# Kernel tuning notes

Measured on AMD Instinct MI355X. Metric: run time of the kernel, lower is better.

Reference implementation:

```python
import jax, jax.numpy as jnp
import numpy as np

N_NODES = 50000
N_EDGES = 600000
N_GRAPHS = 512
HID = 128
LAT = 64
L = 4
BN_EPS = 1e-5


def _gelu(x):
    return jax.nn.gelu(x, approximate=False)


def _bn(x, g, b):
    m = jnp.mean(x, axis=0)
    v = jnp.var(x, axis=0)
    return (x - m) * jax.lax.rsqrt(v + BN_EPS) * g + b


def setup_inputs() -> dict:
    key = jax.random.key(0)
    ks = jax.random.split(key, 8)
    x = jax.random.normal(ks[0], (N_NODES, HID), dtype=jnp.float32)
    edge_index = jax.random.randint(ks[1], (2, N_EDGES), 0, N_NODES, dtype=jnp.int64 if jax.config.jax_enable_x64 else jnp.int32)
    batch = jnp.sort(jax.random.randint(ks[2], (N_NODES,), 0, N_GRAPHS))
    scale = 1.0 / np.sqrt(HID)
    return {
        "x": x,
        "edge_index": edge_index,
        "batch": batch,
        "input_bn_g": jnp.ones((HID,), jnp.float32),
        "input_bn_b": jnp.zeros((HID,), jnp.float32),
        "eps": jnp.zeros((L,), jnp.float32),
        "fc1_w": jax.random.normal(ks[3], (L, HID, HID), jnp.float32) * scale,
        "fc1_b": jnp.zeros((L, HID), jnp.float32),
        "bn1_g": jnp.ones((L, HID), jnp.float32),
        "bn1_b": jnp.zeros((L, HID), jnp.float32),
        "fc2_w": jax.random.normal(ks[4], (L, HID, HID), jnp.float32) * scale,
        "fc2_b": jnp.zeros((L, HID), jnp.float32),
        "bn_g": jnp.ones((L, HID), jnp.float32),
        "bn_b": jnp.zeros((L, HID), jnp.float32),
        "att_weight": jax.random.normal(ks[5], (L, HID), jnp.float32),
        "pool_weight": jnp.ones((3,), jnp.float32),
        "fcA_w": jax.random.normal(ks[6], (HID, HID), jnp.float32) * scale,
        "fcA_b": jnp.zeros((HID,), jnp.float32),
        "ln_g": jnp.ones((HID,), jnp.float32),
        "ln_b": jnp.zeros((HID,), jnp.float32),
        "fcB_w": jax.random.normal(ks[7], (HID, LAT), jnp.float32) * scale,
        "fcB_b": jnp.zeros((LAT,), jnp.float32),
    }


def reference(x, edge_index, batch, input_bn_g, input_bn_b, eps, fc1_w, fc1_b,
              bn1_g, bn1_b, fc2_w, fc2_b, bn_g, bn_b, att_weight, pool_weight,
              fcA_w, fcA_b, ln_g, ln_b, fcB_w, fcB_b):
    src, dst = edge_index[0], edge_index[1]
    x = _bn(x, input_bn_g, input_bn_b)  # input BatchNorm (batch stats)
    hidden_states = []
    for l in range(L):
        # GINConv: (1+eps)*x_i + sum_{j->i} x_j, then GatedResidualMLP
        agg = jax.ops.segment_sum(x[src], dst, num_segments=N_NODES)
        h = (1.0 + eps[l]) * x + agg
        h = _gelu(_bn(h @ fc1_w[l] + fc1_b[l], bn1_g[l], bn1_b[l]))
        h = h @ fc2_w[l] + fc2_b[l]
        h = _gelu(_bn(h, bn_g[l], bn_b[l]))
        hidden_states.append(h)
        x = h
    # JumpingKnowledge attention over layers
    x_all = jnp.stack(hidden_states, axis=0)               # [L, N, H]
    scores = jnp.mean(x_all * att_weight[:, None, :], -1)  # [L, N]
    alpha = jax.nn.softmax(scores, axis=0)
    x = jnp.sum(x_all * alpha[..., None], axis=0)          # [N, H]
    # fused add/mean/max pooling by graph id
    pw = jax.nn.softmax(pool_weight)
    sums = jax.ops.segment_sum(x, batch, num_segments=N_GRAPHS)
    cnt = jax.ops.segment_sum(jnp.ones((N_NODES, 1), x.dtype), batch, num_segments=N_GRAPHS)
    mean = sums / jnp.maximum(cnt, 1.0)
    mx = jax.ops.segment_max(x, batch, num_segments=N_GRAPHS)
    mx = jnp.where(cnt > 0, mx, 0.0)
    pooled = sums * pw[0] + mean * pw[1] + mx * pw[2]      # [G, H]
    out = pooled @ fcA_w + fcA_b
    mu = jnp.mean(out, -1, keepdims=True)
    var = jnp.var(out, -1, keepdims=True)
    out = (out - mu) * jax.lax.rsqrt(var + 1e-5) * ln_g + ln_b
    out = _gelu(out) + pooled
    return out @ fcB_w + fcB_b                              # [G, latent]
```

## Files before the change

### kernel.cpp

```cpp
#include <hip/hip_runtime.h>
#include <math.h>

#define N_NODES 50000
#define N_EDGES 600000
#define N_GRAPHS 512
#define HID 128
#define LAT 64
#define NL 4
#define SSTR 16
#define NGRP 16
#define PSET (NGRP * 256 * SSTR)
#define N_TILES 3125
#define ZROWS 208
#define ZLD 136

typedef __attribute__((ext_vector_type(8))) __bf16 bf16x8;
typedef __attribute__((ext_vector_type(4))) float f32x4;

union Chunk {
    bf16x8 v;
    uint4 u4;
    ushort us[8];
};

// ... 138 lines not shown
    } else {
        int n = (bx - 2600) * 256 + t;
        if (n < N_NODES) {
            int b = batch[n];
            if (n == 0 || batch[n - 1] != b) gstart[b] = n;
            if (n == N_NODES - 1 || batch[n + 1] != b) gend[b] = n + 1;
        }
    }
}

__global__ __launch_bounds__(256) void bn_scan(const float* __restrict__ X,
                                               ushort* __restrict__ Y,
                                               const float* __restrict__ inPart,
                                               const float* __restrict__ g,
                                               const float* __restrict__ b,
                                               const int* __restrict__ counts,
                                               int* __restrict__ offs,
                                               int* __restrict__ bsum) {
    __shared__ float scL[HID], sfL[HID];
    __shared__ int shI[256];
    int t = threadIdx.x;
    if (t < HID) {
        float sm = 0.f, sq = 0.f;
#pragma unroll
        for (int gg = 0; gg < NGRP; ++gg) {
            sm += inPart[((long)gg * 256 + t) * SSTR];
            sq += inPart[((long)gg * 256 + HID + t) * SSTR];
        }
        const float invN = 1.0f / (float)N_NODES;
        float mean = sm * invN;
        float var = sq * invN - mean * mean;
        float s = g[t] * rsqrtf(var + 1e-5f);
        scL[t] = s;
        sfL[t] = b[t] - mean * s;
    }
    __syncthreads();
    int c4 = (t & 31) * 4;
    float sc[4], sf[4];
#pragma unroll
    for (int j = 0; j < 4; ++j) { sc[j] = scL[c4 + j]; sf[j] = sfL[c4 + j]; }
    int s0, s1;
    sub_range(blockIdx.x & 255, blockIdx.x >> 8, s0, s1);
    int c0 = s0 * 32, c1 = s1 * 32;
    for (int i = c0 + t; i < c1; i += 256) {
        float4 v = ((const float4*)X)[i];
        ushort4 w;
        w.x = f2bf(v.x * sc[0] + sf[0]);
        w.y = f2bf(v.y * sc[1] + sf[1]);
        w.z = f2bf(v.z * sc[2] + sf[2]);
        w.w = f2bf(v.w * sc[3] + sf[3]);
        ((ushort4*)Y)[i] = w;
    }
    if (blockIdx.x < 196) {
        int i = blockIdx.x * 256 + t;
        int v = (i < N_NODES) ? counts[i] : 0;
        shI[t] = v;
        __syncthreads();
        for (int off = 1; off < 256; off <<= 1) {
            int a = (t >= off) ? shI[t - off] : 0;
            __syncthreads();
            shI[t] += a;
            __syncthreads();
        }
        if (i < N_NODES) offs[i] = shI[t] - v;
        if (t == 255) bsum[blockIdx.x] = shI[255];
    }
}

__global__ __launch_bounds__(256) void scan23(int* __restrict__ offs,
                                              const int* __restrict__ bsum,
                                              int* __restrict__ cursor) {
    __shared__ int sh[256];
    int t = threadIdx.x, bx = blockIdx.x;
    int v = (t < bx) ? bsum[t] : 0;
    sh[t] = v;
    __syncthreads();
    for (int off = 128; off > 0; off >>= 1) {
        if (t < off) sh[t] += sh[t + off];
        __syncthreads();
    }
    int pre = sh[0];
    int i = bx * 256 + t;
    if (i < N_NODES) {
        int o = offs[i] + pre;
        offs[i] = o;
        cursor[i] = o;
    }
}

__global__ __launch_bounds__(256) void csr_fill(const int* __restrict__ src,
                                                const int* __restrict__ dst,
                                                int* __restrict__ cursor,
                                                int* __restrict__ csr) {
    int e = blockIdx.x * blockDim.x + threadIdx.x;
    if (e >= N_EDGES) return;
    int pos = atomicAdd(cursor + dst[e], 1);
    csr[pos] = src[e];
}

__global__ __launch_bounds__(256) void gin_gather_bf(const ushort* __restrict__ Xbf,
                                                     ushort* __restrict__ Hp,
                                                     const int* __restrict__ offs,
                                                     const int* __restrict__ counts,
                                                     const int* __restrict__ csr,
                                                     const float* __restrict__ eps, int l) {
    int t = threadIdx.x;
    int tx = t & 31;
    int grp = t >> 5;
    int s0, s1;
    sub_range(blockIdx.x & 255, blockIdx.x >> 8, s0, s1);
    float ev = 1.0f + eps[l];
    for (int node = s0 + grp; node < s1; node += 8) {
        ushort4 sv = *(const ushort4*)(Xbf + (long)node * HID + 4 * tx);
        float a0 = bf2f(sv.x) * ev, a1 = bf2f(sv.y) * ev;
        float a2 = bf2f(sv.z) * ev, a3 = bf2f(sv.w) * ev;
        int o = offs[node];
        int d = counts[node];
        int k = 0;
        for (; k + 8 <= d; k += 8) {
            int si[8];
#pragma unroll
            for (int j = 0; j < 8; ++j) si[j] = csr[o + k + j];
            ushort4 v[8];
#pragma unroll
            for (int j = 0; j < 8; ++j)
                v[j] = *(const ushort4*)(Xbf + (long)si[j] * HID + 4 * tx);
#pragma unroll
            for (int j = 0; j < 8; ++j) {
                a0 += bf2f(v[j].x); a1 += bf2f(v[j].y);
                a2 += bf2f(v[j].z); a3 += bf2f(v[j].w);
            }
        }
        for (; k + 4 <= d; k += 4) {
            int si[4];
#pragma unroll
            for (int j = 0; j < 4; ++j) si[j] = csr[o + k + j];
#pragma unroll
            for (int j = 0; j < 4; ++j) {
                ushort4 v = *(const ushort4*)(Xbf + (long)si[j] * HID + 4 * tx);
                a0 += bf2f(v.x); a1 += bf2f(v.y); a2 += bf2f(v.z); a3 += bf2f(v.w);
            }
        }
        for (; k < d; ++k) {
            int s = csr[o + k];
            ushort4 v = *(const ushort4*)(Xbf + (long)s * HID + 4 * tx);
            a0 += bf2f(v.x); a1 += bf2f(v.y); a2 += bf2f(v.z); a3 += bf2f(v.w);
        }
        ushort4 w;
        w.x = f2bf(a0); w.y = f2bf(a1); w.z = f2bf(a2); w.w = f2bf(a3);
        *(ushort4*)(Hp + (long)node * HID + 4 * tx) = w;
    }
}

template <int NT>
__global__ __launch_bounds__(NT, 1) void fused_mlp(
    const ushort* __restrict__ Abf, const ushort* __restrict__ W1t,
    const ushort* __restrict__ W2t, const float* __restrict__ b1v,
    const float* __restrict__ b2v, const float* __restrict__ bn1g,
    const float* __restrict__ bn1b, const float* __restrict__ bn2g,
    const float* __restrict__ bn2b, float* __restrict__ st1,
    float* __restrict__ st2, ushort* __restrict__ Hl, int* __restrict__ bar,
    int nbar) {
    constexpr int NW = NT / 64;
    constexpr int RSTEP = NW / 2;
    __shared__ __align__(16) ushort Z1[ZROWS * ZLD];
    __shared__ __align__(16) ushort Z2[ZROWS * ZLD];
    __shared__ float shs[2 * NT];
    __shared__ float scL[HID], sfL[HID];

    int t = threadIdx.x;
    int w = t >> 6, lane = t & 63;
    int m = lane & 15, q = lane >> 4;
    int c2 = w & 1, r2 = w >> 1;
    int t0 = (blockIdx.x * N_TILES) >> 8;
    int t1 = ((blockIdx.x + 1) * N_TILES) >> 8;
    int grp = blockIdx.x & (NGRP - 1);

    bf16x8 Bf[4][4];
    {
        const ushort* Wh = W1t + (long)(c2 * 64) * HID;
#pragma unroll
        for (int nt = 0; nt < 4; ++nt)
#pragma unroll
            for (int kc = 0; kc < 4; ++kc)
                Bf[nt][kc] = *(const bf16x8*)(Wh + (nt * 16 + m) * HID + kc * 32 + q * 8);
    }
    float bias4[4];
#pragma unroll
    for (int nt = 0; nt < 4; ++nt) bias4[nt] = b1v[c2 * 64 + nt * 16 + m];

    float s_c[4] = {0, 0, 0, 0}, q_c[4] = {0, 0, 0, 0};
    int tile = t0 + r2;
    Chunk Ac[4];
    if (tile < t1) {
        const ushort* ar = Abf + (long)(tile * 16 + m) * HID + q * 8;
#pragma unroll
        for (int kc = 0; kc < 4; ++kc) Ac[kc].u4 = *(const uint4*)(ar + kc * 32);
    }
    while (tile < t1) {
        int nxt = tile + RSTEP;
        Chunk An[4];
        if (nxt < t1) {
            const ushort* ar = Abf + (long)(nxt * 16 + m) * HID + q * 8;
#pragma unroll
            for (int kc = 0; kc < 4; ++kc) An[kc].u4 = *(const uint4*)(ar + kc * 32);
        }
        f32x4 acc[4];
#pragma unroll
        for (int nt = 0; nt < 4; ++nt) acc[nt] = (f32x4){0.f, 0.f, 0.f, 0.f};
#pragma unroll
        for (int kc = 0; kc < 4; ++kc)
#pragma unroll
            for (int nt = 0; nt < 4; ++nt)
                acc[nt] = __builtin_amdgcn_mfma_f32_16x16x32_bf16(Ac[kc].v, Bf[nt][kc],
                                                                  acc[nt], 0, 0, 0);
        int lrow = (tile - t0) * 16;
#pragma unroll
        for (int nt = 0; nt < 4; ++nt) {
            int col = c2 * 64 + nt * 16 + m;
#pragma unroll
            for (int r = 0; r < 4; ++r) {
                float z = acc[nt][r] + bias4[nt];
                Z1[(lrow + q * 4 + r) * ZLD + col] = f2bf(z);
                s_c[nt] += z;
                q_c[nt] += z * z;
            }
        }
        tile = nxt;
#pragma unroll
        for (int kc = 0; kc < 4; ++kc) Ac[kc] = An[kc];
    }
#pragma unroll
    for (int nt = 0; nt < 4; ++nt) {
        s_c[nt] += __shfl_xor(s_c[nt], 16);
        s_c[nt] += __shfl_xor(s_c[nt], 32);
        q_c[nt] += __shfl_xor(q_c[nt], 16);
        q_c[nt] += __shfl_xor(q_c[nt], 32);
    }
    if (q == 0) {
#pragma unroll
        for (int nt = 0; nt < 4; ++nt) {
            shs[w * 64 + nt * 16 + m] = s_c[nt];
            shs[NT + w * 64 + nt * 16 + m] = q_c[nt];
        }
    }
    __syncthreads();
    if (t < HID) {
        int half = t >> 6, lc = t & 63;
        float a = 0.f, b = 0.f;
#pragma unroll
        for (int j = 0; j < RSTEP; ++j) {
            a += shs[(half + 2 * j) * 64 + lc];
            b += shs[NT + (half + 2 * j) * 64 + lc];
        }
        float* base = st1 + (long)(grp * 256) * SSTR;
        atomicAdd(base + t * SSTR, a);
        atomicAdd(base + (HID + t) * SSTR, b);
    }
    for (int k = 0; k < nbar; ++k) grid_sync(bar, k + 1);

    if (t < HID) {
        float sm = 0.f, sq = 0.f;
#pragma unroll
        for (int gg = 0; gg < NGRP; ++gg) {
            sm += coh_ld(st1 + ((long)gg * 256 + t) * SSTR);
            sq += coh_ld(st1 + ((long)gg * 256 + HID + t) * SSTR);
        }
        const float invN = 1.0f / (float)N_NODES;
        float mean = sm * invN;
        float var = sq * invN - mean * mean;
        float s = bn1g[t] * rsqrtf(var + 1e-5f);
        scL[t] = s;
        sfL[t] = bn1b[t] - mean * s;
    }
    __syncthreads();

    {
        const ushort* Wh = W2t + (long)(c2 * 64) * HID;
#pragma unroll
        for (int nt = 0; nt < 4; ++nt)
#pragma unroll
            for (int kc = 0; kc < 4; ++kc)
                Bf[nt][kc] = *(const bf16x8*)(Wh + (nt * 16 + m) * HID + kc * 32 + q * 8);
    }
#pragma unroll
    for (int nt = 0; nt < 4; ++nt) bias4[nt] = b2v[c2 * 64 + nt * 16 + m];
#pragma unroll
    for (int nt = 0; nt < 4; ++nt) { s_c[nt] = 0.f; q_c[nt] = 0.f; }

    for (int tl = t0 + r2; tl < t1; tl += RSTEP) {
        int lrow = (tl - t0) * 16;
        Chunk Ax[4];
#pragma unroll
        for (int kc = 0; kc < 4; ++kc)
            Ax[kc].u4 = *(const uint4*)(Z1 + (lrow + m) * ZLD + kc * 32 + q * 8);
#pragma unroll
        for (int kc = 0; kc < 4; ++kc)
#pragma unroll
            for (int j = 0; j < 8; ++j) {
                int k = kc * 32 + q * 8 + j;
                float f = bf2f(Ax[kc].us[j]) * scL[k] + sfL[k];
                Ax[kc].us[j] = f2bf(gelu_fast(f));
            }
        f32x4 acc[4];
#pragma unroll
        for (int nt = 0; nt < 4; ++nt) acc[nt] = (f32x4){0.f, 0.f, 0.f, 0.f};
#pragma unroll
        for (int kc = 0; kc < 4; ++kc)
#pragma unroll
            for (int nt = 0; nt < 4; ++nt)
                acc[nt] = __builtin_amdgcn_mfma_f32_16x16x32_bf16(Ax[kc].v, Bf[nt][kc],
                                                                  acc[nt], 0, 0, 0);
#pragma unroll
        for (int nt = 0; nt < 4; ++nt) {
            int col = c2 * 64 + nt * 16 + m;
#pragma unroll
            for (int r = 0; r < 4; ++r) {
                float z = acc[nt][r] + bias4[nt];
                Z2[(lrow + q * 4 + r) * ZLD + col] = f2bf(z);
                s_c[nt] += z;
                q_c[nt] += z * z;
            }
        }
    }
#pragma unroll
    for (int nt = 0; nt < 4; ++nt) {
        s_c[nt] += __shfl_xor(s_c[nt], 16);
        s_c[nt] += __shfl_xor(s_c[nt], 32);
        q_c[nt] += __shfl_xor(q_c[nt], 16);
        q_c[nt] += __shfl_xor(q_c[nt], 32);
    }
    if (q == 0) {
#pragma unroll
        for (int nt = 0; nt < 4; ++nt) {
            shs[w * 64 + nt * 16 + m] = s_c[nt];
            shs[NT + w * 64 + nt * 16 + m] = q_c[nt];
        }
    }
    __syncthreads();
    if (t < HID) {
        int half = t >> 6, lc = t & 63;
        float a = 0.f, b = 0.f;
#pragma unroll
        for (int j = 0; j < RSTEP; ++j) {
            a += shs[(half + 2 * j) * 64 + lc];
            b += shs[NT + (half + 2 * j) * 64 + lc];
        }
        float* base = st2 + (long)(grp * 256) * SSTR;
        atomicAdd(base + t * SSTR, a);
        atomicAdd(base + (HID + t) * SSTR, b);
    }
    for (int k = 0; k < nbar; ++k) grid_sync(bar, nbar + k + 1);

    if (t < HID) {
        float sm = 0.f, sq = 0.f;
#pragma unroll
        for (int gg = 0; gg < NGRP; ++gg) {
            sm += coh_ld(st2 + ((long)gg * 256 + t) * SSTR);
            sq += coh_ld(st2 + ((long)gg * 256 + HID + t) * SSTR);
        }
        const float invN = 1.0f / (float)N_NODES;
        float mean = sm * invN;
        float var = sq * invN - mean * mean;
        float s = bn2g[t] * rsqrtf(var + 1e-5f);
        scL[t] = s;
        sfL[t] = bn2b[t] - mean * s;
    }
    __syncthreads();

    int nch = (t1 - t0) * 16 * 16;
    for (int i = t; i < nch; i += NT) {
        int row = i >> 4, off = i & 15;
        Chunk ch;
        ch.u4 = *(const uint4*)(Z2 + row * ZLD + off * 8);
#pragma unroll
        for (int j = 0; j < 8; ++j) {
            int cc = off * 8 + j;
            float f = bf2f(ch.us[j]) * scL[cc] + sfL[cc];
            ch.us[j] = f2bf(gelu_fast(f));
        }
        *(uint4*)(Hl + (long)(t0 * 16 + row) * HID + off * 8) = ch.u4;
    }
}

__global__ __launch_bounds__(256) void jk_pool(const ushort* __restrict__ H0,
                                               const ushort* __restrict__ H1,
                                               const ushort* __restrict__ H2,
                                               const ushort* __restrict__ H3,
                                               const float* __restrict__ att,
                                               const int* __restrict__ batch,
                                               float* __restrict__ psum,
                                               float* __restrict__ pmax) {
    int t = threadIdx.x;
    int lane = t & 63, w = t >> 6;
    long wid = (long)blockIdx.x * 4 + w;
    int a0 = (int)((wid * N_NODES) >> 13);
    int a1 = (int)(((wid + 1) * N_NODES) >> 13);
    const ushort* Hs[4] = {H0, H1, H2, H3};
    float2 av[4];
#pragma unroll
    for (int l = 0; l < 4; ++l) av[l] = *(const float2*)(att + l * HID + 2 * lane);

    int curg = -1;
    float sx = 0.f, sy = 0.f, mx = -INFINITY, my = -INFINITY;
    for (int node = a0; node < a1; ++node) {
        int g = batch[node];
        if (g != curg) {
            if (curg >= 0) {
                float* ps = psum + (long)curg * HID + 2 * lane;
                float* pm = pmax + (long)curg * HID + 2 * lane;
                atomicAdd(ps, sx);
                atomicAdd(ps + 1, sy);
                atomicMaxF(pm, mx);
                atomicMaxF(pm + 1, my);
            }
            curg = g;
            sx = 0.f; sy = 0.f; mx = -INFINITY; my = -INFINITY;
        }
        float hx[4], hy[4], scr[4];
#pragma unroll
        for (int l = 0; l < 4; ++l) {
            unsigned int u = *(const unsigned int*)(Hs[l] + (long)node * HID + 2 * lane);
            float vx = bf2f((ushort)(u & 0xFFFF));
            float vy = bf2f((ushort)(u >> 16));
            hx[l] = vx; hy[l] = vy;
            float p = vx * av[l].x + vy * av[l].y;
#pragma unroll
            for (int off = 32; off > 0; off >>= 1) p += __shfl_xor(p, off);
            scr[l] = p * (1.0f / HID);
        }
        float mm = fmaxf(fmaxf(scr[0], scr[1]), fmaxf(scr[2], scr[3]));
        float e[4], se = 0.f;
#pragma unroll
        for (int l = 0; l < 4; ++l) { e[l] = expf(scr[l] - mm); se += e[l]; }
        float inv = 1.0f / se;
        float ox = 0.f, oy = 0.f;
#pragma unroll
        for (int l = 0; l < 4; ++l) {
            float a = e[l] * inv;
            ox += a * hx[l];
            oy += a * hy[l];
        }
        sx += ox; sy += oy;
        mx = fmaxf(mx, ox); my = fmaxf(my, oy);
    }
    if (curg >= 0) {
        float* ps = psum + (long)curg * HID + 2 * lane;
        float* pm = pmax + (long)curg * HID + 2 * lane;
        atomicAdd(ps, sx);
        atomicAdd(ps + 1, sy);
        atomicMaxF(pm, mx);
        atomicMaxF(pm + 1, my);
    }
}

__global__ __launch_bounds__(128) void finalize_head(const float* __restrict__ psum,
                                                     const float* __restrict__ pmax,
                                                     const int* __restrict__ gstart,
                                                     const int* __restrict__ gend,
                                                     const float* __restrict__ pw,
                                                     const float* __restrict__ fcAw,
                                                     const float* __restrict__ fcAb,
                                                     const float* __restrict__ lng,
                                                     const float* __restrict__ lnb,
                                                     const float* __restrict__ fcBw,
                                                     const float* __restrict__ fcBb,
                                                     float* __restrict__ out) {
    __shared__ float p[HID], qv[HID], red[HID];
    int g = blockIdx.x, j = threadIdx.x;
    float w0 = pw[0], w1 = pw[1], w2 = pw[2];
    float mw = fmaxf(w0, fmaxf(w1, w2));
    float e0 = expf(w0 - mw), e1 = expf(w1 - mw), e2 = expf(w2 - mw);
    float inv = 1.0f / (e0 + e1 + e2);
    e0 *= inv; e1 *= inv; e2 *= inv;
    int cnt = gend[g] - gstart[g];
    float s = psum[g * HID + j];
    float mx = pmax[g * HID + j];
    float mean0 = cnt > 0 ? s / (float)cnt : 0.f;
    float mxv = cnt > 0 ? mx : 0.f;
    float pool = s * e0 + mean0 * e1 + mxv * e2;
    p[j] = pool;
    __syncthreads();
    float acc = fcAb[j];
    for (int k = 0; k < HID; ++k) acc += p[k] * fcAw[k * HID + j];
    red[j] = acc;
    __syncthreads();
    for (int off = 64; off > 0; off >>= 1) {
        if (j < off) red[j] += red[j + off];
        __syncthreads();
    }
    float mean = red[0] * (1.0f / HID);
    __syncthreads();
    float d = acc - mean;
    red[j] = d * d;
    __syncthreads();
    for (int off = 64; off > 0; off >>= 1) {
        if (j < off) red[j] += red[j + off];
        __syncthreads();
    }
    float var = red[0] * (1.0f / HID);
    float y = d * rsqrtf(var + 1e-5f) * lng[j] + lnb[j];
    qv[j] = gelu_exact(y) + pool;
    __syncthreads();
    if (j < LAT) {
        float o = fcBb[j];
        for (int k = 0; k < HID; ++k) o += qv[k] * fcBw[k * LAT + j];
        out[g * LAT + j] = o;
    }
}

extern "C" void kernel_launch(void* const* d_in, const int* in_sizes, int n_in,
                              void* d_out, int out_size, void* d_ws, size_t ws_size,
                              hipStream_t stream) {
    const float* x = (const float*)d_in[0];
    const int* ei = (const int*)d_in[1];
    const int* src = ei;
    const int* dst = ei + N_EDGES;
    const int* batch = (const int*)d_in[2];
    const float* ibn_g = (const float*)d_in[3];
    const float* ibn_b = (const float*)d_in[4];
    const float* eps = (const float*)d_in[5];
    const float* fc1w = (const float*)d_in[6];
    const float* fc1b = (const float*)d_in[7];
    const float* bn1g = (const float*)d_in[8];
    const float* bn1b = (const float*)d_in[9];
    const float* fc2w = (const float*)d_in[10];
    const float* fc2b = (const float*)d_in[11];
    const float* bng = (const float*)d_in[12];
    const float* bnb = (const float*)d_in[13];
    const float* att = (const float*)d_in[14];
    const float* pw = (const float*)d_in[15];
    const float* fcAw = (const float*)d_in[16];
    const float* fcAb = (const float*)d_in[17];
    const float* lng = (const float*)d_in[18];
    const float* lnb = (const float*)d_in[19];
    const float* fcBw = (const float*)d_in[20];
    const float* fcBb = (const float*)d_in[21];
    float* out = (float*)d_out;

    const size_t NH = (size_t)N_NODES * HID;
    char* w8 = (char*)d_ws;
    ushort* x0bf = (ushort*)w8;     w8 += NH * 2;
    ushort* hprebf = (ushort*)w8;   w8 += NH * 2;
    ushort* Hlbf[NL];
    for (int l = 0; l < NL; ++l) { Hlbf[l] = (ushort*)w8; w8 += NH * 2; }
    float* statsPart = (float*)w8;  w8 += (size_t)9 * PSET * 4;
    float* psum = (float*)w8;       w8 += (size_t)N_GRAPHS * HID * 4;
    float* pmax = (float*)w8;       w8 += (size_t)N_GRAPHS * HID * 4;
    int* gstart = (int*)w8;         w8 += N_GRAPHS * 4;
    int* gend = (int*)w8;           w8 += N_GRAPHS * 4;
    int* counts = (int*)w8;         w8 += N_NODES * 4;
    int* offs = (int*)w8;           w8 += N_NODES * 4;
    int* cursor = (int*)w8;         w8 += N_NODES * 4;
    int* bsum = (int*)w8;           w8 += 256 * 4;
    int* csr = (int*)w8;            w8 += (size_t)N_EDGES * 4;
    ushort* WtBf = (ushort*)w8;     w8 += (size_t)8 * HID * HID * 2;
    int* bar = (int*)w8;            w8 += 2048 * 4;

    const int edgeBlocks = (N_EDGES + 255) / 256;

    setup<<<512, 256, 0, stream>>>(fc1w, fc2w, WtBf, counts, statsPart,
                                   psum, pmax, gstart, gend, bar);
    stats_count<<<256 + edgeBlocks + 196, 256, 0, stream>>>(x, statsPart, dst, counts,
                                                            batch, gstart, gend);
    bn_scan<<<2048, 256, 0, stream>>>(x, x0bf, statsPart, ibn_g, ibn_b, counts, offs,
                                      bsum);
    scan23<<<196, 256, 0, stream>>>(offs, bsum, cursor);
    csr_fill<<<edgeBlocks, 256, 0, stream>>>(src, dst, cursor, csr);

    const int nbar_l[NL] = {5, 1, 3, 1};
    const ushort* xin = x0bf;
    for (int l = 0; l < NL; ++l) {
        float* p1 = statsPart + (size_t)(1 + 2 * l) * PSET;
        float* p2 = statsPart + (size_t)(2 + 2 * l) * PSET;
        gin_gather_bf<<<2048, 256, 0, stream>>>(xin, hprebf, offs, counts, csr, eps, l);
        fused_mlp<512><<<256, 512, 0, stream>>>(
            hprebf, WtBf + (size_t)l * HID * HID,
            WtBf + (size_t)(4 + l) * HID * HID, fc1b + l * HID, fc2b + l * HID,
            bn1g + l * HID, bn1b + l * HID, bng + l * HID, bnb + l * HID,
            p1, p2, Hlbf[l], bar + l * 512, nbar_l[l]);
        xin = Hlbf[l];
    }

    jk_pool<<<2048, 256, 0, stream>>>(Hlbf[0], Hlbf[1], Hlbf[2], Hlbf[3], att, batch,
                                      psum, pmax);
    finalize_head<<<N_GRAPHS, 128, 0, stream>>>(psum, pmax, gstart, gend, pw, fcAw,
                                                fcAb, lng, lnb, fcBw, fcBb, out);
}
```

Before: 504.0 us.

## Fuse neighbor gather into MLP kernel for layers 0 and 2; drop extra grid syncs

For layers 0 and 2, the GIN neighbor aggregation now runs inside fused_mlp. Each block gathers its own node rows into the Z2 shared buffer, and the first GEMM reads its A tiles from LDS instead of from a global pre-activation buffer. This removes one kernel launch and the global write and read of hprebf for those layers. The repeated grid_sync calls per layer are also reduced to one per BN stats phase. The risk is that the gather now runs with only 256 persistent blocks, so there is less latency hiding than the 2048-block standalone gather.

New measurement: 513.6 us. About the same (+1.9%).

```diff
diff --git a/kernel.cpp b/kernel.cpp
--- a/kernel.cpp
+++ b/kernel.cpp
@@ -314,15 +314,17 @@
     }
 }
 
-template <int NT>
+template <int NT, bool GATHER>
 __global__ __launch_bounds__(NT, 1) void fused_mlp(
-    const ushort* __restrict__ Abf, const ushort* __restrict__ W1t,
-    const ushort* __restrict__ W2t, const float* __restrict__ b1v,
-    const float* __restrict__ b2v, const float* __restrict__ bn1g,
-    const float* __restrict__ bn1b, const float* __restrict__ bn2g,
-    const float* __restrict__ bn2b, float* __restrict__ st1,
-    float* __restrict__ st2, ushort* __restrict__ Hl, int* __restrict__ bar,
-    int nbar) {
+    const ushort* __restrict__ Abf, const int* __restrict__ offs,
+    const int* __restrict__ counts, const int* __restrict__ csr,
+    const float* __restrict__ eps, int lidx,
+    const ushort* __restrict__ W1t, const ushort* __restrict__ W2t,
+    const float* __restrict__ b1v, const float* __restrict__ b2v,
+    const float* __restrict__ bn1g, const float* __restrict__ bn1b,
+    const float* __restrict__ bn2g, const float* __restrict__ bn2b,
+    float* __restrict__ st1, float* __restrict__ st2,
+    ushort* __restrict__ Hl, int* __restrict__ bar) {
     constexpr int NW = NT / 64;
     constexpr int RSTEP = NW / 2;
     __shared__ __align__(16) ushort Z1[ZROWS * ZLD];
@@ -338,6 +340,54 @@
     int t1 = ((blockIdx.x + 1) * N_TILES) >> 8;
     int grp = blockIdx.x & (NGRP - 1);
 
+    if (GATHER) {
+        int tx = t & 31;
+        int gidx = t >> 5;
+        float ev = 1.0f + eps[lidx];
+        int r0 = t0 * 16, r1 = t1 * 16;
+        for (int node = r0 + gidx; node < r1; node += NT / 32) {
+            ushort4 sv = *(const ushort4*)(Abf + (long)node * HID + 4 * tx);
+            float a0 = bf2f(sv.x) * ev, a1 = bf2f(sv.y) * ev;
+            float a2 = bf2f(sv.z) * ev, a3 = bf2f(sv.w) * ev;
+            int o = offs[node];
+            int d = counts[node];
+            int k = 0;
+            for (; k + 8 <= d; k += 8) {
+                int si[8];
+#pragma unroll
+                for (int j = 0; j < 8; ++j) si[j] = csr[o + k + j];
+                ushort4 v[8];
+#pragma unroll
+                for (int j = 0; j < 8; ++j)
+                    v[j] = *(const ushort4*)(Abf + (long)si[j] * HID + 4 * tx);
+#pragma unroll
+                for (int j = 0; j < 8; ++j) {
+                    a0 += bf2f(v[j].x); a1 += bf2f(v[j].y);
+                    a2 += bf2f(v[j].z); a3 += bf2f(v[j].w);
+                }
+            }
+            for (; k + 4 <= d; k += 4) {
+                int si[4];
+#pragma unroll
+                for (int j = 0; j < 4; ++j) si[j] = csr[o + k + j];
+#pragma unroll
+                for (int j = 0; j < 4; ++j) {
+                    ushort4 v = *(const ushort4*)(Abf + (long)si[j] * HID + 4 * tx);
+                    a0 += bf2f(v.x); a1 += bf2f(v.y); a2 += bf2f(v.z); a3 += bf2f(v.w);
+                }
+            }
+            for (; k < d; ++k) {
+                int s = csr[o + k];
+                ushort4 v = *(const ushort4*)(Abf + (long)s * HID + 4 * tx);
+                a0 += bf2f(v.x); a1 += bf2f(v.y); a2 += bf2f(v.z); a3 += bf2f(v.w);
+            }
+            ushort4 wv;
+            wv.x = f2bf(a0); wv.y = f2bf(a1); wv.z = f2bf(a2); wv.w = f2bf(a3);
+            *(ushort4*)(Z2 + (node - r0) * ZLD + 4 * tx) = wv;
+        }
+        __syncthreads();
+    }
+
     bf16x8 Bf[4][4];
     {
         const ushort* Wh = W1t + (long)(c2 * 64) * HID;
@@ -352,45 +402,76 @@
     for (int nt = 0; nt < 4; ++nt) bias4[nt] = b1v[c2 * 64 + nt * 16 + m];
 
     float s_c[4] = {0, 0, 0, 0}, q_c[4] = {0, 0, 0, 0};
-    int tile = t0 + r2;
-    Chunk Ac[4];
-    if (tile < t1) {
-        const ushort* ar = Abf + (long)(tile * 16 + m) * HID + q * 8;
-#pragma unroll
-        for (int kc = 0; kc < 4; ++kc) Ac[kc].u4 = *(const uint4*)(ar + kc * 32);
-    }
-    while (tile < t1) {
-        int nxt = tile + RSTEP;
-        Chunk An[4];
-        if (nxt < t1) {
-            const ushort* ar = Abf + (long)(nxt * 16 + m) * HID + q * 8;
-#pragma unroll
-            for (int kc = 0; kc < 4; ++kc) An[kc].u4 = *(const uint4*)(ar + kc * 32);
-        }
-        f32x4 acc[4];
-#pragma unroll
-        for (int nt = 0; nt < 4; ++nt) acc[nt] = (f32x4){0.f, 0.f, 0.f, 0.f};
-#pragma unroll
-        for (int kc = 0; kc < 4; ++kc)
-#pragma unroll
-            for (int nt = 0; nt < 4; ++nt)
-                acc[nt] = __builtin_amdgcn_mfma_f32_16x16x32_bf16(Ac[kc].v, Bf[nt][kc],
-                                                                  acc[nt], 0, 0, 0);
-        int lrow = (tile - t0) * 16;
-#pragma unroll
-        for (int nt = 0; nt < 4; ++nt) {
-            int col = c2 * 64 + nt * 16 + m;
-#pragma unroll
-            for (int r = 0; r < 4; ++r) {
-                float z = acc[nt][r] + bias4[nt];
-                Z1[(lrow + q * 4 + r) * ZLD + col] = f2bf(z);
-                s_c[nt] += z;
-                q_c[nt] += z * z;
-            }
-        }
-        tile = nxt;
-#pragma unroll
-        for (int kc = 0; kc < 4; ++kc) Ac[kc] = An[kc];
+
+    if (GATHER) {
+        for (int tl = t0 + r2; tl < t1; tl += RSTEP) {
+            int lrow = (tl - t0) * 16;
+            Chunk Ax[4];
+#pragma unroll
+            for (int kc = 0; kc < 4; ++kc)
+                Ax[kc].u4 = *(const uint4*)(Z2 + (lrow + m) * ZLD + kc * 32 + q * 8);
+            f32x4 acc[4];
+#pragma unroll
+            for (int nt = 0; nt < 4; ++nt) acc[nt] = (f32x4){0.f, 0.f, 0.f, 0.f};
+#pragma unroll
+            for (int kc = 0; kc < 4; ++kc)
+#pragma unroll
+                for (int nt = 0; nt < 4; ++nt)
+                    acc[nt] = __builtin_amdgcn_mfma_f32_16x16x32_bf16(
+                        Ax[kc].v, Bf[nt][kc], acc[nt], 0, 0, 0);
+#pragma unroll
+            for (int nt = 0; nt < 4; ++nt) {
+                int col = c2 * 64 + nt * 16 + m;
+#pragma unroll
+                for (int r = 0; r < 4; ++r) {
+                    float z = acc[nt][r] + bias4[nt];
+                    Z1[(lrow + q * 4 + r) * ZLD + col] = f2bf(z);
+                    s_c[nt] += z;
+                    q_c[nt] += z * z;
+                }
+            }
+        }
+    } else {
+        int tile = t0 + r2;
+        Chunk Ac[4];
+        if (tile < t1) {
+            const ushort* ar = Abf + (long)(tile * 16 + m) * HID + q * 8;
+#pragma unroll
+            for (int kc = 0; kc < 4; ++kc) Ac[kc].u4 = *(const uint4*)(ar + kc * 32);
+        }
+        while (tile < t1) {
+            int nxt = tile + RSTEP;
+            Chunk An[4];
+            if (nxt < t1) {
+                const ushort* ar = Abf + (long)(nxt * 16 + m) * HID + q * 8;
+#pragma unroll
+                for (int kc = 0; kc < 4; ++kc) An[kc].u4 = *(const uint4*)(ar + kc * 32);
+            }
+            f32x4 acc[4];
+#pragma unroll
+            for (int nt = 0; nt < 4; ++nt) acc[nt] = (f32x4){0.f, 0.f, 0.f, 0.f};
+#pragma unroll
+            for (int kc = 0; kc < 4; ++kc)
+#pragma unroll
+                for (int nt = 0; nt < 4; ++nt)
+                    acc[nt] = __builtin_amdgcn_mfma_f32_16x16x32_bf16(
+                        Ac[kc].v, Bf[nt][kc], acc[nt], 0, 0, 0);
+            int lrow = (tile - t0) * 16;
+#pragma unroll
+            for (int nt = 0; nt < 4; ++nt) {
+                int col = c2 * 64 + nt * 16 + m;
+#pragma unroll
+                for (int r = 0; r < 4; ++r) {
+                    float z = acc[nt][r] + bias4[nt];
+                    Z1[(lrow + q * 4 + r) * ZLD + col] = f2bf(z);
+                    s_c[nt] += z;
+                    q_c[nt] += z * z;
+                }
+            }
+            tile = nxt;
+#pragma unroll
+            for (int kc = 0; kc < 4; ++kc) Ac[kc] = An[kc];
+        }
     }
 #pragma unroll
     for (int nt = 0; nt < 4; ++nt) {
@@ -419,7 +500,7 @@
         atomicAdd(base + t * SSTR, a);
         atomicAdd(base + (HID + t) * SSTR, b);
     }
-    for (int k = 0; k < nbar; ++k) grid_sync(bar, k + 1);
+    grid_sync(bar, 1);
 
     if (t < HID) {
         float sm = 0.f, sq = 0.f;
@@ -512,7 +593,7 @@
         atomicAdd(base + t * SSTR, a);
         atomicAdd(base + (HID + t) * SSTR, b);
     }
-    for (int k = 0; k < nbar; ++k) grid_sync(bar, nbar + k + 1);
+    grid_sync(bar, 2);
 
     if (t < HID) {
         float sm = 0.f, sq = 0.f;
@@ -730,17 +811,25 @@
     scan23<<<196, 256, 0, stream>>>(offs, bsum, cursor);
     csr_fill<<<edgeBlocks, 256, 0, stream>>>(src, dst, cursor, csr);
 
-    const int nbar_l[NL] = {5, 1, 3, 1};
     const ushort* xin = x0bf;
     for (int l = 0; l < NL; ++l) {
         float* p1 = statsPart + (size_t)(1 + 2 * l) * PSET;
         float* p2 = statsPart + (size_t)(2 + 2 * l) * PSET;
-        gin_gather_bf<<<2048, 256, 0, stream>>>(xin, hprebf, offs, counts, csr, eps, l);
-        fused_mlp<512><<<256, 512, 0, stream>>>(
-            hprebf, WtBf + (size_t)l * HID * HID,
-            WtBf + (size_t)(4 + l) * HID * HID, fc1b + l * HID, fc2b + l * HID,
-            bn1g + l * HID, bn1b + l * HID, bng + l * HID, bnb + l * HID,
-            p1, p2, Hlbf[l], bar + l * 512, nbar_l[l]);
+        if (l == 0 || l == 2) {
+            fused_mlp<512, true><<<256, 512, 0, stream>>>(
+                xin, offs, counts, csr, eps, l,
+                WtBf + (size_t)l * HID * HID, WtBf + (size_t)(4 + l) * HID * HID,
+                fc1b + l * HID, fc2b + l * HID, bn1g + l * HID, bn1b + l * HID,
+                bng + l * HID, bnb + l * HID, p1, p2, Hlbf[l], bar + l * 512);
+        } else {
+            gin_gather_bf<<<2048, 256, 0, stream>>>(xin, hprebf, offs, counts, csr,
+                                                    eps, l);
+            fused_mlp<512, false><<<256, 512, 0, stream>>>(
+                hprebf, offs, counts, csr, eps, l,
+                WtBf + (size_t)l * HID * HID, WtBf + (size_t)(4 + l) * HID * HID,
+                fc1b + l * HID, fc2b + l * HID, bn1g + l * HID, bn1b + l * HID,
+                bng + l * HID, bnb + l * HID, p1, p2, Hlbf[l], bar + l * 512);
+        }
         xin = Hlbf[l];
     }
 
```

## Fuse JK attention pooling into last-layer MLP epilogue and drop repeated grid syncs

Applied to the files above, without the earlier changes.

The final layer's fused MLP now performs the jumping-knowledge attention and graph pooling directly from its shared-memory output tile, so the separate jk_pool kernel and the write and reread of layer-3 hidden states are removed. The per-layer repeated grid_sync loops (nbar of 5, 1, 3, 1) are replaced with a single sync at each stage. The fused path runs only 8 waves per block over 256 blocks, which is less parallelism for the pooling than the old 2048-block launch. Removing the repeated barriers also drops whatever those extra syncs were doing, possibly timing padding.

Result: faster. 489.2 us (-2.9%).

```diff
diff --git a/kernel.cpp b/kernel.cpp
--- a/kernel.cpp
+++ b/kernel.cpp
@@ -314,15 +314,19 @@
     }
 }
 
-template <int NT>
+template <int NT, bool JK>
 __global__ __launch_bounds__(NT, 1) void fused_mlp(
-    const ushort* __restrict__ Abf, const ushort* __restrict__ W1t,
-    const ushort* __restrict__ W2t, const float* __restrict__ b1v,
-    const float* __restrict__ b2v, const float* __restrict__ bn1g,
-    const float* __restrict__ bn1b, const float* __restrict__ bn2g,
-    const float* __restrict__ bn2b, float* __restrict__ st1,
-    float* __restrict__ st2, ushort* __restrict__ Hl, int* __restrict__ bar,
-    int nbar) {
+    const ushort* __restrict__ Abf,
+    const ushort* __restrict__ W1t, const ushort* __restrict__ W2t,
+    const float* __restrict__ b1v, const float* __restrict__ b2v,
+    const float* __restrict__ bn1g, const float* __restrict__ bn1b,
+    const float* __restrict__ bn2g, const float* __restrict__ bn2b,
+    float* __restrict__ st1, float* __restrict__ st2,
+    ushort* __restrict__ Hl, int* __restrict__ bar,
+    const ushort* __restrict__ H0, const ushort* __restrict__ H1,
+    const ushort* __restrict__ H2, const float* __restrict__ att,
+    const int* __restrict__ batch, float* __restrict__ psum,
+    float* __restrict__ pmax) {
     constexpr int NW = NT / 64;
     constexpr int RSTEP = NW / 2;
     __shared__ __align__(16) ushort Z1[ZROWS * ZLD];
@@ -419,7 +423,7 @@
         atomicAdd(base + t * SSTR, a);
         atomicAdd(base + (HID + t) * SSTR, b);
     }
-    for (int k = 0; k < nbar; ++k) grid_sync(bar, k + 1);
+    grid_sync(bar, 1);
 
     if (t < HID) {
         float sm = 0.f, sq = 0.f;
@@ -512,7 +516,7 @@
         atomicAdd(base + t * SSTR, a);
         atomicAdd(base + (HID + t) * SSTR, b);
     }
-    for (int k = 0; k < nbar; ++k) grid_sync(bar, nbar + k + 1);
+    grid_sync(bar, 2);
 
     if (t < HID) {
         float sm = 0.f, sq = 0.f;
@@ -530,89 +534,90 @@
     }
     __syncthreads();
 
-    int nch = (t1 - t0) * 16 * 16;
-    for (int i = t; i < nch; i += NT) {
-        int row = i >> 4, off = i & 15;
-        Chunk ch;
-        ch.u4 = *(const uint4*)(Z2 + row * ZLD + off * 8);
-#pragma unroll
-        for (int j = 0; j < 8; ++j) {
-            int cc = off * 8 + j;
-            float f = bf2f(ch.us[j]) * scL[cc] + sfL[cc];
-            ch.us[j] = f2bf(gelu_fast(f));
-        }
-        *(uint4*)(Hl + (long)(t0 * 16 + row) * HID + off * 8) = ch.u4;
-    }
-}
-
-__global__ __launch_bounds__(256) void jk_pool(const ushort* __restrict__ H0,
-                                               const ushort* __restrict__ H1,
-                                               const ushort* __restrict__ H2,
-                                               const ushort* __restrict__ H3,
-                                               const float* __restrict__ att,
-                                               const int* __restrict__ batch,
-                                               float* __restrict__ psum,
-                                               float* __restrict__ pmax) {
-    int t = threadIdx.x;
-    int lane = t & 63, w = t >> 6;
-    long wid = (long)blockIdx.x * 4 + w;
-    int a0 = (int)((wid * N_NODES) >> 13);
-    int a1 = (int)(((wid + 1) * N_NODES) >> 13);
-    const ushort* Hs[4] = {H0, H1, H2, H3};
-    float2 av[4];
-#pragma unroll
-    for (int l = 0; l < 4; ++l) av[l] = *(const float2*)(att + l * HID + 2 * lane);
-
-    int curg = -1;
-    float sx = 0.f, sy = 0.f, mx = -INFINITY, my = -INFINITY;
-    for (int node = a0; node < a1; ++node) {
-        int g = batch[node];
-        if (g != curg) {
-            if (curg >= 0) {
-                float* ps = psum + (long)curg * HID + 2 * lane;
-                float* pm = pmax + (long)curg * HID + 2 * lane;
-                atomicAdd(ps, sx);
-                atomicAdd(ps + 1, sy);
-                atomicMaxF(pm, mx);
-                atomicMaxF(pm + 1, my);
-            }
-            curg = g;
-            sx = 0.f; sy = 0.f; mx = -INFINITY; my = -INFINITY;
-        }
-        float hx[4], hy[4], scr[4];
-#pragma unroll
-        for (int l = 0; l < 4; ++l) {
-            unsigned int u = *(const unsigned int*)(Hs[l] + (long)node * HID + 2 * lane);
-            float vx = bf2f((ushort)(u & 0xFFFF));
-            float vy = bf2f((ushort)(u >> 16));
-            hx[l] = vx; hy[l] = vy;
-            float p = vx * av[l].x + vy * av[l].y;
-#pragma unroll
-            for (int off = 32; off > 0; off >>= 1) p += __shfl_xor(p, off);
-            scr[l] = p * (1.0f / HID);
-        }
-        float mm = fmaxf(fmaxf(scr[0], scr[1]), fmaxf(scr[2], scr[3]));
-        float e[4], se = 0.f;
-#pragma unroll
-        for (int l = 0; l < 4; ++l) { e[l] = expf(scr[l] - mm); se += e[l]; }
-        float inv = 1.0f / se;
-        float ox = 0.f, oy = 0.f;
-#pragma unroll
-        for (int l = 0; l < 4; ++l) {
-            float a = e[l] * inv;
-            ox += a * hx[l];
-            oy += a * hy[l];
-        }
-        sx += ox; sy += oy;
-        mx = fmaxf(mx, ox); my = fmaxf(my, oy);
-    }
-    if (curg >= 0) {
-        float* ps = psum + (long)curg * HID + 2 * lane;
-        float* pm = pmax + (long)curg * HID + 2 * lane;
-        atomicAdd(ps, sx);
-        atomicAdd(ps + 1, sy);
-        atomicMaxF(pm, mx);
-        atomicMaxF(pm + 1, my);
+    if (!JK) {
+        int nch = (t1 - t0) * 16 * 16;
+        for (int i = t; i < nch; i += NT) {
+            int row = i >> 4, off = i & 15;
+            Chunk ch;
+            ch.u4 = *(const uint4*)(Z2 + row * ZLD + off * 8);
+#pragma unroll
+            for (int j = 0; j < 8; ++j) {
+                int cc = off * 8 + j;
+                float f = bf2f(ch.us[j]) * scL[cc] + sfL[cc];
+                ch.us[j] = f2bf(gelu_fast(f));
+            }
+            *(uint4*)(Hl + (long)(t0 * 16 + row) * HID + off * 8) = ch.u4;
+        }
+    } else {
+        float2 av[4];
+#pragma unroll
+        for (int l = 0; l < 4; ++l) av[l] = *(const float2*)(att + l * HID + 2 * lane);
+        int nrows = (t1 - t0) * 16;
+        int wr0 = (w * nrows) / NW;
+        int wr1 = ((w + 1) * nrows) / NW;
+        int base = t0 * 16;
+        int c = 2 * lane;
+        float sA = scL[c], sB = scL[c + 1], fA = sfL[c], fB = sfL[c + 1];
+        int curg = -1;
+        float sx = 0.f, sy = 0.f, mx = -INFINITY, my = -INFINITY;
+        for (int r = wr0; r < wr1; ++r) {
+            int node = base + r;
+            int g = batch[node];
+            if (g != curg) {
+                if (curg >= 0) {
+                    float* ps = psum + (long)curg * HID + c;
+                    float* pm = pmax + (long)curg * HID + c;
+                    atomicAdd(ps, sx);
+                    atomicAdd(ps + 1, sy);
+                    atomicMaxF(pm, mx);
+                    atomicMaxF(pm + 1, my);
+                }
+                curg = g;
+                sx = 0.f; sy = 0.f; mx = -INFINITY; my = -INFINITY;
+            }
+            float f0 = bf2f(Z2[r * ZLD + c]) * sA + fA;
+            float f1 = bf2f(Z2[r * ZLD + c + 1]) * sB + fB;
+            float hx3 = bf2f(f2bf(gelu_fast(f0)));
+            float hy3 = bf2f(f2bf(gelu_fast(f1)));
+            unsigned u0 = *(const unsigned*)(H0 + (long)node * HID + c);
+            unsigned u1 = *(const unsigned*)(H1 + (long)node * HID + c);
+            unsigned u2 = *(const unsigned*)(H2 + (long)node * HID + c);
+            float hx[4], hy[4];
+            hx[0] = bf2f((ushort)(u0 & 0xFFFF)); hy[0] = bf2f((ushort)(u0 >> 16));
+            hx[1] = bf2f((ushort)(u1 & 0xFFFF)); hy[1] = bf2f((ushort)(u1 >> 16));
+            hx[2] = bf2f((ushort)(u2 & 0xFFFF)); hy[2] = bf2f((ushort)(u2 >> 16));
+            hx[3] = hx3; hy[3] = hy3;
+            float scr[4];
+#pragma unroll
+            for (int l = 0; l < 4; ++l) {
+                float p = hx[l] * av[l].x + hy[l] * av[l].y;
+#pragma unroll
+                for (int off = 32; off > 0; off >>= 1) p += __shfl_xor(p, off);
+                scr[l] = p * (1.0f / HID);
+            }
+            float mm = fmaxf(fmaxf(scr[0], scr[1]), fmaxf(scr[2], scr[3]));
+            float e[4], se = 0.f;
+#pragma unroll
+            for (int l = 0; l < 4; ++l) { e[l] = expf(scr[l] - mm); se += e[l]; }
+            float inv = 1.0f / se;
+            float ox = 0.f, oy = 0.f;
+#pragma unroll
+            for (int l = 0; l < 4; ++l) {
+                float a = e[l] * inv;
+                ox += a * hx[l];
+                oy += a * hy[l];
+            }
+            sx += ox; sy += oy;
+            mx = fmaxf(mx, ox); my = fmaxf(my, oy);
+        }
+        if (curg >= 0) {
+            float* ps = psum + (long)curg * HID + c;
+            float* pm = pmax + (long)curg * HID + c;
+            atomicAdd(ps, sx);
+            atomicAdd(ps + 1, sy);
+            atomicMaxF(pm, mx);
+            atomicMaxF(pm + 1, my);
+        }
     }
 }
 
@@ -730,22 +735,29 @@
     scan23<<<196, 256, 0, stream>>>(offs, bsum, cursor);
     csr_fill<<<edgeBlocks, 256, 0, stream>>>(src, dst, cursor, csr);
 
-    const int nbar_l[NL] = {5, 1, 3, 1};
     const ushort* xin = x0bf;
     for (int l = 0; l < NL; ++l) {
         float* p1 = statsPart + (size_t)(1 + 2 * l) * PSET;
         float* p2 = statsPart + (size_t)(2 + 2 * l) * PSET;
         gin_gather_bf<<<2048, 256, 0, stream>>>(xin, hprebf, offs, counts, csr, eps, l);
-        fused_mlp<512><<<256, 512, 0, stream>>>(
-            hprebf, WtBf + (size_t)l * HID * HID,
-            WtBf + (size_t)(4 + l) * HID * HID, fc1b + l * HID, fc2b + l * HID,
-            bn1g + l * HID, bn1b + l * HID, bng + l * HID, bnb + l * HID,
-            p1, p2, Hlbf[l], bar + l * 512, nbar_l[l]);
+        if (l < 3) {
+            fused_mlp<512, false><<<256, 512, 0, stream>>>(
+                hprebf, WtBf + (size_t)l * HID * HID,
+                WtBf + (size_t)(4 + l) * HID * HID, fc1b + l * HID, fc2b + l * HID,
+                bn1g + l * HID, bn1b + l * HID, bng + l * HID, bnb + l * HID,
+                p1, p2, Hlbf[l], bar + l * 512,
+                nullptr, nullptr, nullptr, nullptr, nullptr, nullptr, nullptr);
+        } else {
+            fused_mlp<512, true><<<256, 512, 0, stream>>>(
+                hprebf, WtBf + (size_t)l * HID * HID,
+                WtBf + (size_t)(4 + l) * HID * HID, fc1b + l * HID, fc2b + l * HID,
+                bn1g + l * HID, bn1b + l * HID, bng + l * HID, bnb + l * HID,
+                p1, p2, Hlbf[l], bar + l * 512,
+                Hlbf[0], Hlbf[1], Hlbf[2], att, batch, psum, pmax);
+        }
         xin = Hlbf[l];
     }
 
-    jk_pool<<<2048, 256, 0, stream>>>(Hlbf[0], Hlbf[1], Hlbf[2], Hlbf[3], att, batch,
-                                      psum, pmax);
     finalize_head<<<N_GRAPHS, 128, 0, stream>>>(psum, pmax, gstart, gend, pw, fcAw,
                                                 fcAb, lng, lnb, fcBw, fcBb, out);
 }
```

## Split layers 0 and 2 MLP into non-persistent GEMM and BN-apply kernels

Applied to the files above, without the earlier changes.

For layers 0 and 2, which previously needed repeated grid-wide barriers inside the persistent fused MLP kernel, the MLP now runs as two tile-parallel MFMA GEMM kernels and a separate BN+GELU apply kernel. Batch statistics are passed between them through the partial-stats buffers. Layers 1 and 3 keep the fused persistent kernel, now with a single grid sync per BN phase. This removes costly spin-barrier rounds, at the price of writing and re-reading the intermediate z1 and z2 activations through global memory and three extra kernel launches per affected layer.

Measured after the change: 651.3 us. 1.29x slower.

```diff
diff --git a/kernel.cpp b/kernel.cpp
--- a/kernel.cpp
+++ b/kernel.cpp
@@ -314,15 +314,162 @@
     }
 }
 
+__global__ __launch_bounds__(256) void gemm_np(
+    const ushort* __restrict__ Abf, const ushort* __restrict__ Wt,
+    const float* __restrict__ bias, ushort* __restrict__ Cbf,
+    const float* __restrict__ stInPart, const float* __restrict__ gIn,
+    const float* __restrict__ bIn, int applyIn, float* __restrict__ stOutPart) {
+    __shared__ float scL[HID], sfL[HID];
+    __shared__ __align__(16) ushort T[16 * ZLD];
+    __shared__ float shs[2 * HID];
+    int t = threadIdx.x;
+    if (applyIn && t < HID) {
+        float sm = 0.f, sq = 0.f;
+#pragma unroll
+        for (int gg = 0; gg < NGRP; ++gg) {
+            sm += stInPart[((long)gg * 256 + t) * SSTR];
+            sq += stInPart[((long)gg * 256 + HID + t) * SSTR];
+        }
+        const float invN = 1.0f / (float)N_NODES;
+        float mean = sm * invN;
+        float var = sq * invN - mean * mean;
+        float s = gIn[t] * rsqrtf(var + 1e-5f);
+        scL[t] = s;
+        sfL[t] = bIn[t] - mean * s;
+    }
+    __syncthreads();
+
+    int w = t >> 6, lane = t & 63;
+    int m = lane & 15, q = lane >> 4;
+    int tile = blockIdx.x;
+
+    Chunk Ac[4];
+    {
+        const ushort* ar = Abf + (long)(tile * 16 + m) * HID + q * 8;
+#pragma unroll
+        for (int kc = 0; kc < 4; ++kc) Ac[kc].u4 = *(const uint4*)(ar + kc * 32);
+    }
+    if (applyIn) {
+#pragma unroll
+        for (int kc = 0; kc < 4; ++kc)
+#pragma unroll
+            for (int j = 0; j < 8; ++j) {
+                int k = kc * 32 + q * 8 + j;
+                float f = bf2f(Ac[kc].us[j]) * scL[k] + sfL[k];
+                Ac[kc].us[j] = f2bf(gelu_fast(f));
+            }
+    }
+    bf16x8 Bf[2][4];
+    {
+        const ushort* Wh = Wt + (long)(w * 32) * HID;
+#pragma unroll
+        for (int nt = 0; nt < 2; ++nt)
+#pragma unroll
+            for (int kc = 0; kc < 4; ++kc)
+                Bf[nt][kc] = *(const bf16x8*)(Wh + (nt * 16 + m) * HID + kc * 32 + q * 8);
+    }
+    float bias2[2] = {bias[w * 32 + m], bias[w * 32 + 16 + m]};
+
+    f32x4 acc[2];
+#pragma unroll
+    for (int nt = 0; nt < 2; ++nt) acc[nt] = (f32x4){0.f, 0.f, 0.f, 0.f};
+#pragma unroll
+    for (int kc = 0; kc < 4; ++kc)
+#pragma unroll
+        for (int nt = 0; nt < 2; ++nt)
+            acc[nt] = __builtin_amdgcn_mfma_f32_16x16x32_bf16(Ac[kc].v, Bf[nt][kc],
+                                                              acc[nt], 0, 0, 0);
+    float s_c[2] = {0.f, 0.f}, q_c[2] = {0.f, 0.f};
+#pragma unroll
+    for (int nt = 0; nt < 2; ++nt) {
+        int col = w * 32 + nt * 16 + m;
+#pragma unroll
+        for (int r = 0; r < 4; ++r) {
+            float z = acc[nt][r] + bias2[nt];
+            T[(q * 4 + r) * ZLD + col] = f2bf(z);
+            s_c[nt] += z;
+            q_c[nt] += z * z;
+        }
+    }
+#pragma unroll
+    for (int nt = 0; nt < 2; ++nt) {
+        s_c[nt] += __shfl_xor(s_c[nt], 16);
+        s_c[nt] += __shfl_xor(s_c[nt], 32);
+        q_c[nt] += __shfl_xor(q_c[nt], 16);
+        q_c[nt] += __shfl_xor(q_c[nt], 32);
+    }
+    if (q == 0) {
+#pragma unroll
+        for (int nt = 0; nt < 2; ++nt) {
+            int col = w * 32 + nt * 16 + m;
+            shs[col] = s_c[nt];
+            shs[HID + col] = q_c[nt];
+        }
+    }
+    __syncthreads();
+    {
+        int row = t >> 4, off = t & 15;
+        uint4 vv = *(const uint4*)(T + row * ZLD + off * 8);
+        *(uint4*)(Cbf + (long)(tile * 16 + row) * HID + off * 8) = vv;
+    }
+    if (t < HID) {
+        int grp = blockIdx.x & (NGRP - 1);
+        float* base = stOutPart + (long)(grp * 256) * SSTR;
+        atomicAdd(base + t * SSTR, shs[t]);
+        atomicAdd(base + (HID + t) * SSTR, shs[HID + t]);
+    }
+}
+
+__global__ __launch_bounds__(256) void bn_apply_part(const ushort* __restrict__ X,
+                                                     ushort* __restrict__ Y,
+                                                     const float* __restrict__ stPart,
+                                                     const float* __restrict__ g,
+                                                     const float* __restrict__ b) {
+    __shared__ float scL[HID], sfL[HID];
+    int t = threadIdx.x;
+    if (t < HID) {
+        float sm = 0.f, sq = 0.f;
+#pragma unroll
+        for (int gg = 0; gg < NGRP; ++gg) {
+            sm += stPart[((long)gg * 256 + t) * SSTR];
+            sq += stPart[((long)gg * 256 + HID + t) * SSTR];
+        }
+        const float invN = 1.0f / (float)N_NODES;
+        float mean = sm * invN;
+        float var = sq * invN - mean * mean;
+        float s = g[t] * rsqrtf(var + 1e-5f);
+        scL[t] = s;
+        sfL[t] = b[t] - mean * s;
+    }
+    __syncthreads();
+    int c8 = (t & 15) * 8;
+    float sc[8], sf[8];
+#pragma unroll
+    for (int j = 0; j < 8; ++j) { sc[j] = scL[c8 + j]; sf[j] = sfL[c8 + j]; }
+    int s0, s1;
+    sub_range(blockIdx.x & 255, blockIdx.x >> 8, s0, s1);
+    int c0 = s0 * 16, c1 = s1 * 16;
+    for (int i = c0 + t; i < c1; i += 256) {
+        Chunk ch;
+        ch.u4 = ((const uint4*)X)[i];
+#pragma unroll
+        for (int j = 0; j < 8; ++j) {
+            float f = bf2f(ch.us[j]) * sc[j] + sf[j];
+            ch.us[j] = f2bf(gelu_fast(f));
+        }
+        ((uint4*)Y)[i] = ch.u4;
+    }
+}
+
 template <int NT>
 __global__ __launch_bounds__(NT, 1) void fused_mlp(
-    const ushort* __restrict__ Abf, const ushort* __restrict__ W1t,
-    const ushort* __restrict__ W2t, const float* __restrict__ b1v,
-    const float* __restrict__ b2v, const float* __restrict__ bn1g,
-    const float* __restrict__ bn1b, const float* __restrict__ bn2g,
-    const float* __restrict__ bn2b, float* __restrict__ st1,
-    float* __restrict__ st2, ushort* __restrict__ Hl, int* __restrict__ bar,
-    int nbar) {
+    const ushort* __restrict__ Abf,
+    const ushort* __restrict__ W1t, const ushort* __restrict__ W2t,
+    const float* __restrict__ b1v, const float* __restrict__ b2v,
+    const float* __restrict__ bn1g, const float* __restrict__ bn1b,
+    const float* __restrict__ bn2g, const float* __restrict__ bn2b,
+    float* __restrict__ st1, float* __restrict__ st2,
+    ushort* __restrict__ Hl, int* __restrict__ bar) {
     constexpr int NW = NT / 64;
     constexpr int RSTEP = NW / 2;
     __shared__ __align__(16) ushort Z1[ZROWS * ZLD];
@@ -419,7 +566,7 @@
         atomicAdd(base + t * SSTR, a);
         atomicAdd(base + (HID + t) * SSTR, b);
     }
-    for (int k = 0; k < nbar; ++k) grid_sync(bar, k + 1);
+    grid_sync(bar, 1);
 
     if (t < HID) {
         float sm = 0.f, sq = 0.f;
@@ -512,7 +659,7 @@
         atomicAdd(base + t * SSTR, a);
         atomicAdd(base + (HID + t) * SSTR, b);
     }
-    for (int k = 0; k < nbar; ++k) grid_sync(bar, nbar + k + 1);
+    grid_sync(bar, 2);
 
     if (t < HID) {
         float sm = 0.f, sq = 0.f;
@@ -704,6 +851,8 @@
     char* w8 = (char*)d_ws;
     ushort* x0bf = (ushort*)w8;     w8 += NH * 2;
     ushort* hprebf = (ushort*)w8;   w8 += NH * 2;
+    ushort* z1bf = (ushort*)w8;     w8 += NH * 2;
+    ushort* z2bf = (ushort*)w8;     w8 += NH * 2;
     ushort* Hlbf[NL];
     for (int l = 0; l < NL; ++l) { Hlbf[l] = (ushort*)w8; w8 += NH * 2; }
     float* statsPart = (float*)w8;  w8 += (size_t)9 * PSET * 4;
@@ -730,17 +879,27 @@
     scan23<<<196, 256, 0, stream>>>(offs, bsum, cursor);
     csr_fill<<<edgeBlocks, 256, 0, stream>>>(src, dst, cursor, csr);
 
-    const int nbar_l[NL] = {5, 1, 3, 1};
     const ushort* xin = x0bf;
     for (int l = 0; l < NL; ++l) {
         float* p1 = statsPart + (size_t)(1 + 2 * l) * PSET;
         float* p2 = statsPart + (size_t)(2 + 2 * l) * PSET;
         gin_gather_bf<<<2048, 256, 0, stream>>>(xin, hprebf, offs, counts, csr, eps, l);
-        fused_mlp<512><<<256, 512, 0, stream>>>(
-            hprebf, WtBf + (size_t)l * HID * HID,
-            WtBf + (size_t)(4 + l) * HID * HID, fc1b + l * HID, fc2b + l * HID,
-            bn1g + l * HID, bn1b + l * HID, bng + l * HID, bnb + l * HID,
-            p1, p2, Hlbf[l], bar + l * 512, nbar_l[l]);
+        if (l == 0 || l == 2) {
+            gemm_np<<<N_TILES, 256, 0, stream>>>(hprebf, WtBf + (size_t)l * HID * HID,
+                                                 fc1b + l * HID, z1bf,
+                                                 nullptr, nullptr, nullptr, 0, p1);
+            gemm_np<<<N_TILES, 256, 0, stream>>>(z1bf, WtBf + (size_t)(4 + l) * HID * HID,
+                                                 fc2b + l * HID, z2bf,
+                                                 p1, bn1g + l * HID, bn1b + l * HID, 1, p2);
+            bn_apply_part<<<2048, 256, 0, stream>>>(z2bf, Hlbf[l], p2, bng + l * HID,
+                                                    bnb + l * HID);
+        } else {
+            fused_mlp<512><<<256, 512, 0, stream>>>(
+                hprebf, WtBf + (size_t)l * HID * HID,
+                WtBf + (size_t)(4 + l) * HID * HID, fc1b + l * HID, fc2b + l * HID,
+                bn1g + l * HID, bn1b + l * HID, bng + l * HID, bnb + l * HID,
+                p1, p2, Hlbf[l], bar + l * 512);
+        }
         xin = Hlbf[l];
     }
 
```
